# Optimization experiments

Hardware: AMD Instinct MI355X
Metric: run time of the kernel (lower is better)

The kernel has to match this reference:

```python
import jax, jax.numpy as jnp
import numpy as np

B, S, V, H = 1, 2048, 1024, 16
D = V // H  # head_size = 64


def setup_inputs() -> dict:
    key = jax.random.key(0)
    ks = jax.random.split(key, 7)
    s = 1.0 / np.sqrt(V)  # keep logits in a sane range
    return {
        "x": jax.random.normal(ks[0], (B, S, V), jnp.float32),
        "W_qkv": (jax.random.normal(ks[1], (3 * V, V), jnp.float32) * s),
        "W_out": (jax.random.normal(ks[2], (V, V), jnp.float32) * s),
        "W_pos": (jax.random.normal(ks[3], (V, V), jnp.float32) * s),
        "u_vec": (jax.random.normal(ks[4], (1, H, 1, D), jnp.float32) * 0.02),
        "v_vec": (jax.random.normal(ks[5], (1, H, 1, D), jnp.float32) * 0.02),
        "rel_embed": jax.random.normal(ks[6], (S, V), jnp.float32),
    }


def reference(x, W_qkv, W_out, W_pos, u_vec, v_vec, rel_embed):
    b, s, _ = x.shape
    # qkv projection (nn.Linear, no bias): x @ W.T, then split into q,k,v
    qkv = x @ W_qkv.T
    q, k, v = jnp.split(qkv, 3, axis=-1)
    to_heads = lambda t: t.reshape(b, s, H, D).transpose(0, 2, 1, 3)  # [B,H,S,D]
    q, k, v = to_heads(q), to_heads(k), to_heads(v)

    # content term: (q + u) @ k^T  -> [B,H,S,S]
    attn_dots = jnp.einsum('bhid,bhjd->bhij', q + u_vec, k)

    # relative-position term: Linear(rel_embed).T viewed as [H, D, S]
    rel = (rel_embed @ W_pos.T).T.reshape(H, D, s)
    query_posn = jnp.einsum('bhid,hdj->bhij', q + v_vec, rel)  # [B,H,S,S]

    # Transformer-XL style shift-gather: out[i, j] = in[i, (j - i - 1) mod S]
    col_idx = ((-jnp.arange(s))[:, None] + jnp.arange(s)[None, :] - 1) % s
    shifted = jnp.take_along_axis(query_posn, col_idx[None, None, :, :], axis=-1)

    causal_mask = jnp.triu(jnp.ones((s, s), dtype=bool), k=1)  # True above diagonal
    dots = jnp.where(causal_mask, -jnp.inf, attn_dots + shifted) / np.sqrt(D)
    scores = jax.nn.softmax(dots, axis=-1)

    attn = jnp.einsum('bhij,bhjd->bhid', scores, v)
    out = attn.transpose(0, 2, 1, 3).reshape(b, s, V) @ W_out.T
    return out
```

## Files before the change

### kernel.cpp

```cpp
#include <hip/hip_runtime.h>
#include <math.h>

#define S 2048
#define H 16
#define D 64
#define V 1024

typedef float f32x4 __attribute__((ext_vector_type(4)));
typedef __bf16 bf16x8 __attribute__((ext_vector_type(8)));
typedef unsigned short u16;

#define GLOBAL_AS __attribute__((address_space(1)))
#define LDS_AS __attribute__((address_space(3)))

__device__ __forceinline__ u16 f2bf(float x) {
    unsigned u = __float_as_uint(x);
    u = u + 0x7FFFu + ((u >> 16) & 1u);
    return (u16)(u >> 16);
}
__device__ __forceinline__ float bf2f(u16 b) {
    return __uint_as_float(((unsigned)b) << 16);
}

#if __has_builtin(__builtin_amdgcn_global_load_lds)
#define HAS_ASYNC 1
#endif

__device__ __forceinline__ void async_ld16(const u16* g, u16* ldsu, int lane) {
#ifdef HAS_ASYNC
    auto gp = reinterpret_cast<GLOBAL_AS void*>(reinterpret_cast<uintptr_t>(g));
    auto lp = reinterpret_cast<LDS_AS void*>(reinterpret_cast<uintptr_t>(ldsu));
    __builtin_amdgcn_global_load_lds(gp, lp, 16, 0, 0);
#else
    *(uint4*)((char*)ldsu + lane * 16) = *(const uint4*)g;
#endif
}

__global__ __launch_bounds__(256) void prep5(
    const float* __restrict__ a0, u16* __restrict__ b0, int n0,
    const float* __restrict__ a1, u16* __restrict__ b1, int n1,
    const float* __restrict__ a2, u16* __restrict__ b2, int n2,
    const float* __restrict__ a3, u16* __restrict__ b3, int n3,
    const float* __restrict__ a4, u16* __restrict__ b4, int n4)
{
    const int tot = n0 + n1 + n2 + n3 + n4;
    for (int i = blockIdx.x * 256 + threadIdx.x; i < tot; i += gridDim.x * 256) {
        const float* s; u16* d; int j = i;
        if (j < n0) { s = a0; d = b0; }
        else if ((j -= n0) < n1) { s = a1; d = b1; }
        else if ((j -= n1) < n2) { s = a2; d = b2; }
        else if ((j -= n2) < n3) { s = a3; d = b3; }
        else { j -= n3; s = a4; d = b4; }
        float4 f = ((const float4*)s)[j];
        ((ushort4*)d)[j] = make_ushort4(f2bf(f.x), f2bf(f.y), f2bf(f.z), f2bf(f.w));
    }
}

__global__ __launch_bounds__(256) void gemm_proj(
    const u16* __restrict__ x_h, const u16* __restrict__ rel_h,
    const u16* __restrict__ Wq_h, const u16* __restrict__ Wpos_h,
    u16* __restrict__ qk_h, u16* __restrict__ Vt_g, u16* __restrict__ P_h)
{
    __shared__ u16 A_s[2][128 * 64];
    __shared__ u16 B_s[2][128 * 64];

    const int bid = blockIdx.x;
    const bool g1 = bid < 384;
    const int m0 = (g1 ? (bid / 24) : ((bid - 384) / 8)) * 128;
    const int n0 = (g1 ? (bid % 24) : ((bid - 384) % 8)) * 128;
    const u16* Ag = g1 ? x_h : rel_h;
    const u16* Bg = g1 ? Wq_h : Wpos_h;

    const int tid = threadIdx.x;
    const int lane = tid & 63;
    const int w = tid >> 6;
    const int wm = (w & 1) * 64, wn = (w >> 1) * 64;
    const int fr = lane & 15;
    const int fq = lane >> 4;
    const int sr = lane >> 3;
    const int scl = ((lane & 7) ^ sr) * 8;

    auto stage = [&](int k0, int b) {
#pragma unroll
        for (int i = 0; i < 4; ++i) {
            const int r0 = w * 32 + i * 8;
            async_ld16(Ag + (size_t)(m0 + r0 + sr) * 1024 + k0 + scl, A_s[b] + r0 * 64, lane);
            async_ld16(Bg + (size_t)(n0 + r0 + sr) * 1024 + k0 + scl, B_s[b] + r0 * 64, lane);
        }
    };

    f32x4 acc[4][4] = {};

    stage(0, 0);
    for (int kt = 0; kt < 16; ++kt) {
        __syncthreads();
        if (kt + 1 < 16) stage((kt + 1) * 64, (kt + 1) & 1);
        const u16* As = A_s[kt & 1];
        const u16* Bs = B_s[kt & 1];
#pragma unroll
        for (int c = 0; c < 2; ++c) {
            const int ps = ((c * 4 + fq) ^ (fr & 7)) * 8;
            bf16x8 a[4], b[4];
#pragma unroll
            for (int t = 0; t < 4; ++t) {
                a[t] = *(const bf16x8*)&As[(wm + t * 16 + fr) * 64 + ps];
                b[t] = *(const bf16x8*)&Bs[(wn + t * 16 + fr) * 64 + ps];
            }
#pragma unroll
            for (int mi = 0; mi < 4; ++mi)
#pragma unroll
                for (int ni = 0; ni < 4; ++ni)
                    acc[mi][ni] = __builtin_amdgcn_mfma_f32_16x16x32_bf16(
                        a[mi], b[ni], acc[mi][ni], 0, 0, 0);
        }
    }

    const int er = fq * 4;
    if (g1 && n0 >= 2048) {
#pragma unroll
        for (int mi = 0; mi < 4; ++mi)
#pragma unroll
            for (int ni = 0; ni < 4; ++ni) {
                const int col = n0 - 2048 + wn + ni * 16 + fr;
                const int mrow = m0 + wm + mi * 16 + er;
                *(ushort4*)&Vt_g[(size_t)col * 2048 + mrow] = make_ushort4(
                    f2bf(acc[mi][ni][0]), f2bf(acc[mi][ni][1]),
                    f2bf(acc[mi][ni][2]), f2bf(acc[mi][ni][3]));
            }
    } else {
        u16* Cb = g1 ? qk_h : P_h;
        const int ldc = g1 ? 2048 : 1024;
#pragma unroll
        for (int mi = 0; mi < 4; ++mi)
#pragma unroll
            for (int ni = 0; ni < 4; ++ni)
#pragma unroll
                for (int g = 0; g < 4; ++g)
                    Cb[(size_t)(m0 + wm + mi * 16 + er + g) * ldc + n0 + wn + ni * 16 + fr] =
                        f2bf(acc[mi][ni][g]);
    }
}

__global__ __launch_bounds__(256, 3) void attn_mfma(
    const u16* __restrict__ qk_h, const u16* __restrict__ Vt_g,
    const u16* __restrict__ P_h,
    const float* __restrict__ u_vec, const float* __restrict__ v_vec,
    u16* __restrict__ O_h)
{
    const int h = blockIdx.y;
    const int tile = ((blockIdx.y >> 3) & 1) ? blockIdx.x : (gridDim.x - 1 - blockIdx.x);
    const int i0 = tile * 64;
    const int tid = threadIdx.x;
    const int lane = tid & 63;
    const int w = tid >> 6;
    const int fr = lane & 15;
    const int fq = lane >> 4;

    __shared__ u16 K_s[64 * 72];
    __shared__ u16 Vt_s[64 * 72];
    __shared__ u16 P_s[2][64 * 72];
    __shared__ u16 p_s[64 * 72];

    bf16x8 qu[2], qv[2];
    {
        const int row = i0 + w * 16 + fr;
        const int base = h * 64 + fq * 8;
#pragma unroll
        for (int c = 0; c < 2; ++c) {
            bf16x8 q8 = *(const bf16x8*)(qk_h + (size_t)row * 2048 + base + c * 32);
            float4 u0 = *(const float4*)(u_vec + base + c * 32);
            float4 u1 = *(const float4*)(u_vec + base + c * 32 + 4);
            float4 v0 = *(const float4*)(v_vec + base + c * 32);
            float4 v1 = *(const float4*)(v_vec + base + c * 32 + 4);
            const float uf[8] = {u0.x, u0.y, u0.z, u0.w, u1.x, u1.y, u1.z, u1.w};
            const float vf[8] = {v0.x, v0.y, v0.z, v0.w, v1.x, v1.y, v1.z, v1.w};
#pragma unroll
            for (int j = 0; j < 8; ++j) {
                const float qf = (float)q8[j];
                qu[c][j] = (__bf16)(qf + uf[j]);
                qv[c][j] = (__bf16)(qf + vf[j]);
            }
        }
    }

    const int rKV = tid >> 2;
    const int cKV = (tid & 3) * 16;
    const int rP = tid >> 2;
    const int cP = (tid & 3) * 16;

    uint4 pfK0, pfK1, pfV0, pfV1, pfP0, pfP1;
    auto load_pf = [&](int j0) {
        const u16* kg = qk_h + (size_t)(j0 + rKV) * 2048 + 1024 + h * 64 + cKV;
        pfK0 = *(const uint4*)kg;
        pfK1 = *(const uint4*)(kg + 8);
        const u16* vg = Vt_g + (size_t)(h * 64 + rKV) * 2048 + j0 + cKV;
        pfV0 = *(const uint4*)vg;
        pfV1 = *(const uint4*)(vg + 8);
        int prow = S + j0 - i0 + rP;
        if (prow > S - 1) prow = S - 1;
        const u16* pg = P_h + (size_t)prow * 1024 + h * 64 + cP;
        pfP0 = *(const uint4*)pg;
        pfP1 = *(const uint4*)(pg + 8);
    };

    {
        const int prow = S - i0 - 64 + rP;
        const u16* pg = P_h + (size_t)prow * 1024 + h * 64 + cP;
        *(uint4*)&P_s[0][rP * 72 + cP] = *(const uint4*)pg;
        *(uint4*)&P_s[0][rP * 72 + cP + 8] = *(const uint4*)(pg + 8);
    }

    u16* Pcur = P_s[0];
    u16* Pnxt = P_s[1];

    f32x4 O[4] = {};
    float l[4] = {};

    const int tbase = 3 - w;
    const int bsh = 15 - fq * 4;

    load_pf(0);

    for (int j0 = 0; j0 <= i0; j0 += 64) {
        __syncthreads();
        *(uint4*)&K_s[rKV * 72 + cKV] = pfK0;
        *(uint4*)&K_s[rKV * 72 + cKV + 8] = pfK1;
        *(uint4*)&Vt_s[rKV * 72 + cKV] = pfV0;
        *(uint4*)&Vt_s[rKV * 72 + cKV + 8] = pfV1;
        *(uint4*)&Pnxt[rP * 72 + cP] = pfP0;
        *(uint4*)&Pnxt[rP * 72 + cP + 8] = pfP1;
        __syncthreads();
        if (j0 + 64 <= i0) load_pf(j0 + 64);

        f32x4 accQK[4] = {};
        f32x4 accQP[5] = {};
#pragma unroll
        for (int c = 0; c < 2; ++c) {
            const int kk = c * 32 + fq * 8;
#pragma unroll
            for (int nt = 0; nt < 4; ++nt) {
                bf16x8 b = *(const bf16x8*)&K_s[(nt * 16 + fr) * 72 + kk];
                accQK[nt] = __builtin_amdgcn_mfma_f32_16x16x32_bf16(qu[c], b, accQK[nt], 0, 0, 0);
            }
#pragma unroll
            for (int t = 0; t < 5; ++t) {
                const int s = tbase + t;
                const u16* Pb = (s < 4) ? Pcur : Pnxt;
                bf16x8 b = *(const bf16x8*)&Pb[((s & 3) * 16 + fr) * 72 + kk];
                accQP[t] = __builtin_amdgcn_mfma_f32_16x16x32_bf16(qv[c], b, accQP[t], 0, 0, 0);
            }
        }

        float p[4][4];
#pragma unroll
        for (int nt = 0; nt < 4; ++nt)
#pragma unroll
            for (int g = 0; g < 4; ++g) {
                const int b = bsh - g;
                const int srcLane = (fq << 4) | ((fr + b) & 15);
                const float sv = (fr >= b) ? accQP[nt][g] : accQP[nt + 1][g];
                const float qp = __shfl(sv, srcLane, 64);
                const int rr = w * 16 + fq * 4 + g;
                const int j = nt * 16 + fr;
                const float s = (accQK[nt][g] + qp) * 0.125f;
                const float e = ((j0 + j) <= (i0 + rr)) ? __expf(s) : 0.f;
                p[nt][g] = e;
                l[g] += e;
            }
#pragma unroll
        for (int nt = 0; nt < 4; ++nt)
#pragma unroll
            for (int g = 0; g < 4; ++g)
                p_s[(w * 16 + fq * 4 + g) * 72 + nt * 16 + fr] = f2bf(p[nt][g]);

#pragma unroll
        for (int c = 0; c < 2; ++c) {
            const int kk = c * 32 + fq * 8;
            bf16x8 a = *(const bf16x8*)&p_s[(w * 16 + fr) * 72 + kk];
#pragma unroll
            for (int nt = 0; nt < 4; ++nt) {
                bf16x8 b = *(const bf16x8*)&Vt_s[(nt * 16 + fr) * 72 + kk];
                O[nt] = __builtin_amdgcn_mfma_f32_16x16x32_bf16(a, b, O[nt], 0, 0, 0);
            }
        }

        u16* tmp = Pcur; Pcur = Pnxt; Pnxt = tmp;
    }

#pragma unroll
    for (int g = 0; g < 4; ++g)
#pragma unroll
        for (int off = 1; off < 16; off <<= 1)
            l[g] += __shfl_xor(l[g], off, 64);

#pragma unroll
    for (int nt = 0; nt < 4; ++nt)
#pragma unroll
        for (int g = 0; g < 4; ++g) {
            const int rr = w * 16 + fq * 4 + g;
            O_h[(size_t)(i0 + rr) * 1024 + h * 64 + nt * 16 + fr] = f2bf(O[nt][g] / l[g]);
        }
}

__global__ __launch_bounds__(256) void gemm_out(
    const u16* __restrict__ O_g, const u16* __restrict__ Wout_h,
    float* __restrict__ C)
{
    __shared__ u16 A_s[2][64 * 32];
    __shared__ u16 B_s[2][64 * 32];

    const int tid = threadIdx.x;
    const int lane = tid & 63;
    const int w = tid >> 6;
    const int m0 = blockIdx.y * 64, n0 = blockIdx.x * 64;
    const int wm = (w & 1) * 32, wn = (w >> 1) * 32;
    const int fr = lane & 15;
    const int fq = lane >> 4;
    const int lr = lane >> 2, lc = (lane & 3) * 8;

    auto stage = [&](int k0, int bi) {
        async_ld16(O_g + (size_t)(m0 + w * 16 + lr) * 1024 + k0 + lc,
                   A_s[bi] + w * 16 * 32, lane);
        async_ld16(Wout_h + (size_t)(n0 + w * 16 + lr) * 1024 + k0 + lc,
                   B_s[bi] + w * 16 * 32, lane);
    };

    f32x4 acc[2][2] = {};

    stage(0, 0);
    for (int kt = 0; kt < 32; ++kt) {
        __syncthreads();
        if (kt + 1 < 32) stage((kt + 1) * 32, (kt + 1) & 1);
        const u16* As = A_s[kt & 1];
        const u16* Bs = B_s[kt & 1];

        bf16x8 a[2], b[2];
#pragma unroll
        for (int t = 0; t < 2; ++t) {
            a[t] = *(const bf16x8*)&As[(wm + t * 16 + fr) * 32 + fq * 8];
            b[t] = *(const bf16x8*)&Bs[(wn + t * 16 + fr) * 32 + fq * 8];
        }
#pragma unroll
        for (int mi = 0; mi < 2; ++mi)
#pragma unroll
            for (int ni = 0; ni < 2; ++ni)
                acc[mi][ni] = __builtin_amdgcn_mfma_f32_16x16x32_bf16(
                    a[mi], b[ni], acc[mi][ni], 0, 0, 0);
    }

    const int er = fq * 4;
#pragma unroll
    for (int mi = 0; mi < 2; ++mi)
#pragma unroll
        for (int ni = 0; ni < 2; ++ni)
#pragma unroll
            for (int g = 0; g < 4; ++g)
                C[(size_t)(m0 + wm + mi * 16 + er + g) * 1024 + n0 + wn + ni * 16 + fr] =
                    acc[mi][ni][g];
}

extern "C" void kernel_launch(void* const* d_in, const int* in_sizes, int n_in,
                              void* d_out, int out_size, void* d_ws, size_t ws_size,
                              hipStream_t stream) {
    const float* x     = (const float*)d_in[0];
    const float* W_qkv = (const float*)d_in[1];
    const float* W_out = (const float*)d_in[2];
    const float* W_pos = (const float*)d_in[3];
    const float* u_vec = (const float*)d_in[4];
    const float* v_vec = (const float*)d_in[5];
    const float* rel   = (const float*)d_in[6];
    float* out = (float*)d_out;

    char* ws = (char*)d_ws;
    u16* x_h    = (u16*)(ws);
    u16* rel_h  = (u16*)(ws + 4194304);
    u16* Wq_h   = (u16*)(ws + 8388608);
    u16* Wpos_h = (u16*)(ws + 14680064);
    u16* Wout_h = (u16*)(ws + 16777216);
    u16* qk_h   = (u16*)(ws + 18874368);
    u16* Vt_g   = (u16*)(ws + 27262976);
    u16* P_h    = (u16*)(ws + 31457280);
    u16* O_h    = (u16*)(ws + 35651584);

    prep5<<<dim3(2048), dim3(256), 0, stream>>>(
        x, x_h, 2048 * 1024 / 4,
        rel, rel_h, 2048 * 1024 / 4,
        W_qkv, Wq_h, 3072 * 1024 / 4,
        W_pos, Wpos_h, 1024 * 1024 / 4,
        W_out, Wout_h, 1024 * 1024 / 4);

    gemm_proj<<<dim3(512), dim3(256), 0, stream>>>(
        x_h, rel_h, Wq_h, Wpos_h, qk_h, Vt_g, P_h);

    attn_mfma<<<dim3(32, 16), dim3(256), 0, stream>>>(
        qk_h, Vt_g, P_h, u_vec, v_vec, O_h);

    gemm_out<<<dim3(16, 32), dim3(256), 0, stream>>>(O_h, Wout_h, out);
}
```

Before: 181.2 us.

## Double-buffer K/V and triple-buffer P tiles with one barrier per iteration

The attention loop now keeps two LDS buffers for K and V and three rotating buffers for the relative-position tile. Global prefetch runs two tiles ahead, and the next tile's LDS stores happen before the current tile's compute. This removes one of the two __syncthreads per iteration and aims to overlap LDS fills with MFMA work. In exchange, LDS use per block grows substantially and the launch-bounds occupancy hint drops from 3 to 2 blocks, which may reduce latency hiding. A redundant dummy LDS load was also added inside the PV loop.

```diff
diff --git a/kernel.cpp b/kernel.cpp
--- a/kernel.cpp
+++ b/kernel.cpp
@@ -141,7 +141,7 @@
     }
 }
 
-__global__ __launch_bounds__(256, 3) void attn_mfma(
+__global__ __launch_bounds__(256, 2) void attn_mfma(
     const u16* __restrict__ qk_h, const u16* __restrict__ Vt_g,
     const u16* __restrict__ P_h,
     const float* __restrict__ u_vec, const float* __restrict__ v_vec,
@@ -156,9 +156,9 @@
     const int fr = lane & 15;
     const int fq = lane >> 4;
 
-    __shared__ u16 K_s[64 * 72];
-    __shared__ u16 Vt_s[64 * 72];
-    __shared__ u16 P_s[2][64 * 72];
+    __shared__ u16 K_s[2][64 * 72];
+    __shared__ u16 Vt_s[2][64 * 72];
+    __shared__ u16 P_s[3][64 * 72];
     __shared__ u16 p_s[64 * 72];
 
     bf16x8 qu[2], qv[2];
@@ -209,9 +209,18 @@
         *(uint4*)&P_s[0][rP * 72 + cP] = *(const uint4*)pg;
         *(uint4*)&P_s[0][rP * 72 + cP + 8] = *(const uint4*)(pg + 8);
     }
-
-    u16* Pcur = P_s[0];
-    u16* Pnxt = P_s[1];
+    load_pf(0);
+    *(uint4*)&K_s[0][rKV * 72 + cKV] = pfK0;
+    *(uint4*)&K_s[0][rKV * 72 + cKV + 8] = pfK1;
+    *(uint4*)&Vt_s[0][rKV * 72 + cKV] = pfV0;
+    *(uint4*)&Vt_s[0][rKV * 72 + cKV + 8] = pfV1;
+    *(uint4*)&P_s[1][rP * 72 + cP] = pfP0;
+    *(uint4*)&P_s[1][rP * 72 + cP + 8] = pfP1;
+    if (i0 >= 64) load_pf(64);
+
+    u16 *Kcur = K_s[0], *Knxt = K_s[1];
+    u16 *Vcur = Vt_s[0], *Vnxt = Vt_s[1];
+    u16 *Plo = P_s[0], *Phi = P_s[1], *Pwr = P_s[2];
 
     f32x4 O[4] = {};
     float l[4] = {};
@@ -219,18 +228,18 @@
     const int tbase = 3 - w;
     const int bsh = 15 - fq * 4;
 
-    load_pf(0);
+    __syncthreads();
 
     for (int j0 = 0; j0 <= i0; j0 += 64) {
-        __syncthreads();
-        *(uint4*)&K_s[rKV * 72 + cKV] = pfK0;
-        *(uint4*)&K_s[rKV * 72 + cKV + 8] = pfK1;
-        *(uint4*)&Vt_s[rKV * 72 + cKV] = pfV0;
-        *(uint4*)&Vt_s[rKV * 72 + cKV + 8] = pfV1;
-        *(uint4*)&Pnxt[rP * 72 + cP] = pfP0;
-        *(uint4*)&Pnxt[rP * 72 + cP + 8] = pfP1;
-        __syncthreads();
-        if (j0 + 64 <= i0) load_pf(j0 + 64);
+        if (j0 + 64 <= i0) {
+            *(uint4*)&Knxt[rKV * 72 + cKV] = pfK0;
+            *(uint4*)&Knxt[rKV * 72 + cKV + 8] = pfK1;
+            *(uint4*)&Vnxt[rKV * 72 + cKV] = pfV0;
+            *(uint4*)&Vnxt[rKV * 72 + cKV + 8] = pfV1;
+            *(uint4*)&Pwr[rP * 72 + cP] = pfP0;
+            *(uint4*)&Pwr[rP * 72 + cP + 8] = pfP1;
+        }
+        if (j0 + 128 <= i0) load_pf(j0 + 128);
 
         f32x4 accQK[4] = {};
         f32x4 accQP[5] = {};
@@ -239,13 +248,13 @@
             const int kk = c * 32 + fq * 8;
 #pragma unroll
             for (int nt = 0; nt < 4; ++nt) {
-                bf16x8 b = *(const bf16x8*)&K_s[(nt * 16 + fr) * 72 + kk];
+                bf16x8 b = *(const bf16x8*)&Kcur[(nt * 16 + fr) * 72 + kk];
                 accQK[nt] = __builtin_amdgcn_mfma_f32_16x16x32_bf16(qu[c], b, accQK[nt], 0, 0, 0);
             }
 #pragma unroll
             for (int t = 0; t < 5; ++t) {
                 const int s = tbase + t;
-                const u16* Pb = (s < 4) ? Pcur : Pnxt;
+                const u16* Pb = (s < 4) ? Plo : Phi;
                 bf16x8 b = *(const bf16x8*)&Pb[((s & 3) * 16 + fr) * 72 + kk];
                 accQP[t] = __builtin_amdgcn_mfma_f32_16x16x32_bf16(qv[c], b, accQP[t], 0, 0, 0);
             }
@@ -279,12 +288,16 @@
             bf16x8 a = *(const bf16x8*)&p_s[(w * 16 + fr) * 72 + kk];
 #pragma unroll
             for (int nt = 0; nt < 4; ++nt) {
-                bf16x8 b = *(const bf16x8*)&Vt_s[(nt * 16 + fr) * 72 + kk];
+                bf16x8 b = *(const bf16x8*)&Vt_s[0][0];
+                b = *(const bf16x8*)&Vcur[(nt * 16 + fr) * 72 + kk];
                 O[nt] = __builtin_amdgcn_mfma_f32_16x16x32_bf16(a, b, O[nt], 0, 0, 0);
             }
         }
 
-        u16* tmp = Pcur; Pcur = Pnxt; Pnxt = tmp;
+        __syncthreads();
+        { u16* t0 = Kcur; Kcur = Knxt; Knxt = t0; }
+        { u16* t1 = Vcur; Vcur = Vnxt; Vnxt = t1; }
+        { u16* t2 = Plo; Plo = Phi; Phi = Pwr; Pwr = t2; }
     }
 
 #pragma unroll
```

Result: no change. 180.9 us (-0.2%).
